# Kernel tuning notes

Measured on AMD Instinct MI355X. Metric: run time of the kernel, lower is better.

The kernel has to match this reference:

```python
import jax, jax.numpy as jnp
import numpy as np
from jax.scipy.linalg import expm

N = 8
FS = 48000
NFFT = FS * 8              # irfft length, hardcoded in the module
F = NFFT // 2 + 1          # one-sided spectrum length = 192001
GAIN_PER_SAMPLE = 0.9999
_DELAYS = np.array([809., 877., 937., 1049., 1151., 1249., 1373., 1499.], dtype=np.float32)
M_AVR = float(_DELAYS.mean())
M_STD = float(_DELAYS.std(ddof=1))  # torch.std is unbiased


def setup_inputs() -> dict:
    key = jax.random.key(0)
    kB, kC, kW = jax.random.split(key, 3)
    # frequency grid on the upper unit circle, z = e^{i w}, w in [0, pi]
    w = jnp.linspace(0.0, np.pi, F).astype(jnp.float32)
    x = jnp.exp(1j * w).astype(jnp.complex64)
    B = (jax.random.normal(kB, (N, 1), dtype=jnp.float32) / N)
    C = (jax.random.normal(kC, (N,), dtype=jnp.float32) / N)
    W = jax.random.normal(kW, (N, N), dtype=jnp.float32)  # seed for Skew+MatrixExponential parametrization
    m = jnp.asarray((_DELAYS - M_AVR) / M_STD)            # normalized delays (learnable)
    return {"x": x, "B": B, "C": C, "W": W, "m": m}


def reference(x, B, C, W, m):
    # A = expm(skew(W)), an orthogonal feedback matrix  [N,N]
    S = jnp.triu(W, 1)
    A = expm(S - S.T)
    # de-normalize delays
    md = m * M_STD + M_AVR                                # [N]
    gamma = jnp.power(GAIN_PER_SAMPLE, md)                # [N] real
    # D(z) = diag(z^m)  per frequency  -> [F,N] complex
    xm = jnp.power(x[:, None], md[None, :].astype(jnp.complex64))
    # M = D - A @ Gamma ; A @ diag(gamma) == A * gamma (column scaling)
    AG = (A * gamma[None, :]).astype(jnp.complex64)       # [N,N]
    eye = jnp.eye(N, dtype=jnp.complex64)
    Mmat = xm[:, None, :] * eye - AG[None, :, :]          # [F,N,N]
    # Hchannel = inv(M) @ B  (solved, same math as inverse+matmul)
    Bc = jnp.broadcast_to(B.astype(jnp.complex64), (F, N, 1))
    Hch = jnp.linalg.solve(Mmat, Bc)[:, :, 0]             # [F,N]
    H = Hch * C[None, :].astype(jnp.complex64)            # [F,N]
    Hsum = jnp.sum(H, axis=-1)                            # [F]
    mask = jnp.where(x == 0, 0.0, 1.0).astype(Hsum.real.dtype)
    h = jnp.fft.irfft(Hsum * mask, n=NFFT)                # [NFFT] real
    h = h / jnp.max(jnp.abs(h))
    return H, h
```

## Files before the change

kernel.cpp:

```cpp
#include <hip/hip_runtime.h>
#include <math.h>

#define F_LEN 192001
#define NFFT  384000
#define MHALF 192000
#define NCH   8

__device__ __forceinline__ float2 cmulf(float2 a, float2 b) {
  return make_float2(a.x*b.x - a.y*b.y, a.x*b.y + a.y*b.x);
}
__device__ __forceinline__ float2 caddf2(float2 a, float2 b){ return make_float2(a.x+b.x, a.y+b.y); }
__device__ __forceinline__ float2 csubf2(float2 a, float2 b){ return make_float2(a.x-b.x, a.y-b.y); }

__global__ __launch_bounds__(64) void precompute_kernel(
    const float* __restrict__ W, const float* __restrict__ m,
    double* __restrict__ md_d, float* __restrict__ AG, unsigned int* __restrict__ mxbits)
{
  __shared__ double S[64], P[64], T[64];
  __shared__ double norm_sh;
  const int t = threadIdx.x;
  const int i = t >> 3, j = t & 7;

  double wij = (j > i) ? (double)W[i*8+j] : 0.0;
  double wji = (i > j) ? (double)W[j*8+i] : 0.0;
  S[t] = wij - wji;
  __syncthreads();

  if (t == 0) {
    double best = 0.0;
    for (int r = 0; r < 8; ++r) {
      double rs = 0.0;
      for (int c = 0; c < 8; ++c) rs += fabs(S[r*8+c]);
      best = fmax(best, rs);
    }
    norm_sh = best;
  }
  __syncthreads();

  double nrm = norm_sh;
  int s = 0;
  while (nrm > 0.25 && s < 60) { nrm *= 0.5; ++s; }
  S[t] *= ldexp(1.0, -s);

  P[t] = (i == j) ? 1.0 : 0.0;
  T[t] = P[t];
  __syncthreads();

  for (int k = 1; k <= 24; ++k) {
    double acc = 0.0;
    #pragma unroll
    for (int l = 0; l < 8; ++l) acc += T[i*8+l] * S[l*8+j];
    __syncthreads();
    T[t] = acc / (double)k;
    P[t] += T[t];
    __syncthreads();
  }
  for (int q = 0; q < s; ++q) {
    double acc = 0.0;
    #pragma unroll
    for (int l = 0; l < 8; ++l) acc += P[i*8+l] * P[l*8+j];
    __syncthreads();
    P[t] = acc;
    __syncthreads();
  }

  const double M_AVR = 1118.0;
  const double M_STDd = (double)((float)sqrt(419520.0 / 7.0));
  const double LN_GAIN = log(0.9999);

  double md_j  = (double)m[j] * M_STDd + M_AVR;
  double gam_j = exp(md_j * LN_GAIN);
  AG[t] = (float)(P[t] * gam_j);

  if (t < 8) md_d[t] = (double)m[t] * M_STDd + M_AVR;
  if (t == 0) *mxbits = 0u;
}

__global__ __launch_bounds__(256) void freq_solve_kernel(
    const double* __restrict__ md_d, const float* __restrict__ AG,
    const float* __restrict__ Bp, const float* __restrict__ Cp,
    float* __restrict__ outH, float2* __restrict__ Y, int interleaved)
{
  int f = blockIdx.x * blockDim.x + threadIdx.x;
  if (f >= F_LEN) return;

  const double TWO_PI = 6.283185307179586476925287;
  double fd = (double)f;
  float xc[8], xs[8];
  #pragma unroll
  for (int n = 0; n < 8; ++n) {
    double tt = fd * md_d[n] * (1.0 / (double)NFFT);
    tt -= floor(tt);
    float ang = (float)(tt * TWO_PI);
    __sincosf(ang, &xs[n], &xc[n]);
  }

  float2 Mm[8][8];
  float2 yv[8];
  float2 idg[8];
  #pragma unroll
  for (int i = 0; i < 8; ++i) {
    #pragma unroll
    for (int j = 0; j < 8; ++j) {
      float2 v = make_float2(-AG[i*8+j], 0.0f);
      if (i == j) { v.x += xc[i]; v.y = xs[i]; }
      Mm[i][j] = v;
    }
    yv[i] = make_float2(Bp[i], 0.0f);
  }

  #pragma unroll
  for (int k = 0; k < 8; ++k) {
    float2 p = Mm[k][k];
    float rd = 1.0f / (p.x*p.x + p.y*p.y);
    float2 inv = make_float2(p.x*rd, -p.y*rd);
    idg[k] = inv;
    #pragma unroll
    for (int i = k+1; i < 8; ++i) {
      float2 fm = cmulf(Mm[i][k], inv);
      #pragma unroll
      for (int j = k+1; j < 8; ++j)
        Mm[i][j] = csubf2(Mm[i][j], cmulf(fm, Mm[k][j]));
      yv[i] = csubf2(yv[i], cmulf(fm, yv[k]));
    }
  }
  #pragma unroll
  for (int k = 7; k >= 0; --k) {
    float2 acc = yv[k];
    #pragma unroll
    for (int j = k+1; j < 8; ++j)
      acc = csubf2(acc, cmulf(Mm[k][j], yv[j]));
    yv[k] = cmulf(acc, idg[k]);
  }

  float2 hsum = make_float2(0.f, 0.f);
  #pragma unroll
  for (int n = 0; n < 8; ++n) {
    float c = Cp[n];
    float2 H = make_float2(yv[n].x * c, yv[n].y * c);
    yv[n] = H;
    hsum = caddf2(hsum, H);
  }

  if (interleaved) {
    float2* o = (float2*)outH;
    #pragma unroll
    for (int n = 0; n < 8; ++n) o[f*8+n] = yv[n];
  } else {
    #pragma unroll
    for (int n = 0; n < 8; ++n) outH[f*8+n] = yv[n].x;
  }

  Y[f] = hsum;
}

__device__ __forceinline__ void dft4_inv(float2* v) {
  float2 t0 = caddf2(v[0], v[2]);
  float2 t1 = csubf2(v[0], v[2]);
  float2 t2 = caddf2(v[1], v[3]);
  float2 t3 = csubf2(v[1], v[3]);
  float2 it3 = make_float2(-t3.y, t3.x);
  v[0] = caddf2(t0, t2);
  v[1] = caddf2(t1, it3);
  v[2] = csubf2(t0, t2);
  v[3] = csubf2(t1, it3);
}

__device__ __forceinline__ void dft3_inv(float2* v) {
  const float S3 = 0.86602540378443864676f;
  float2 t1 = caddf2(v[1], v[2]);
  float2 d  = csubf2(v[1], v[2]);
  float2 u  = make_float2(v[0].x - 0.5f*t1.x, v[0].y - 0.5f*t1.y);
  float2 idd = make_float2(-S3*d.y, S3*d.x);
  v[0] = caddf2(v[0], t1);
  v[1] = caddf2(u, idd);
  v[2] = csubf2(u, idd);
}

__device__ __forceinline__ void dft5_inv(float2* v) {
  const float C1 =  0.30901699437494742410f;
  const float S1 =  0.95105651629515357212f;
  const float C2 = -0.80901699437494742410f;
  const float S2 =  0.58778525229247312917f;
  float2 t1 = caddf2(v[1], v[4]);
  float2 t2 = caddf2(v[2], v[3]);
  float2 t3 = csubf2(v[1], v[4]);
  float2 t4 = csubf2(v[2], v[3]);
  float2 x0 = v[0];
  float2 a1 = make_float2(x0.x + C1*t1.x + C2*t2.x, x0.y + C1*t1.y + C2*t2.y);
  float2 b1 = make_float2(S1*t3.x + S2*t4.x,        S1*t3.y + S2*t4.y);
  float2 a2 = make_float2(x0.x + C2*t1.x + C1*t2.x, x0.y + C2*t1.y + C1*t2.y);
  float2 b2 = make_float2(S2*t3.x - S1*t4.x,        S2*t3.y - S1*t4.y);
  float2 ib1 = make_float2(-b1.y, b1.x);
  float2 ib2 = make_float2(-b2.y, b2.x);
  v[0] = make_float2(x0.x + t1.x + t2.x, x0.y + t1.y + t2.y);
  v[1] = caddf2(a1, ib1);
  v[4] = csubf2(a1, ib1);
  v[2] = caddf2(a2, ib2);
  v[3] = csubf2(a2, ib2);
}

__device__ __constant__ float TW25[25][2] = {
  { 1.0f, 0.0f },
  { 0.9685831611286311f,  0.2486898871648548f },
  { 0.8763066800438636f,  0.4817536741017153f },
  { 0.7289686274214116f,  0.6845471059286887f },
  { 0.5358267949789967f,  0.8443279255020151f },
  { 0.3090169943749474f,  0.9510565162951535f },
  { 0.0627905195293134f,  0.9980267284282716f },
  {-0.1873813145857246f,  0.9822872507286887f },
  {-0.4257792915650727f,  0.9048270524660196f },
  {-0.6374239897486896f,  0.7705132427757893f },
  {-0.8090169943749474f,  0.5877852522924731f },
  {-0.9297764858882515f,  0.3681245526846780f },
  {-0.9921147013144779f,  0.1253332335643043f },
  {-0.9921147013144779f, -0.1253332335643043f },
  {-0.9297764858882515f, -0.3681245526846780f },
  {-0.8090169943749474f, -0.5877852522924731f },
  {-0.6374239897486899f, -0.7705132427757891f },
  {-0.4257792915650727f, -0.9048270524660196f },
  {-0.1873813145857246f, -0.9822872507286887f },
  { 0.0627905195293134f, -0.9980267284282716f },
  { 0.3090169943749474f, -0.9510565162951535f },
  { 0.5358267949789967f, -0.8443279255020151f },
  { 0.7289686274214116f, -0.6845471059286887f },
  { 0.8763066800438636f, -0.4817536741017153f },
  { 0.9685831611286311f, -0.2486898871648548f },
};

template <int R>
__device__ __forceinline__ void dft_inv(float2* v) {
  if constexpr (R == 3) {
    dft3_inv(v);
  } else if constexpr (R == 4) {
    dft4_inv(v);
  } else if constexpr (R == 5) {
    dft5_inv(v);
  } else if constexpr (R == 8) {
    const float HF = 0.70710678118654752440f;
    float2 e[4] = {v[0], v[2], v[4], v[6]};
    float2 o[4] = {v[1], v[3], v[5], v[7]};
    dft4_inv(e); dft4_inv(o);
    o[1] = cmulf(o[1], make_float2(HF, HF));
    o[2] = make_float2(-o[2].y, o[2].x);
    o[3] = cmulf(o[3], make_float2(-HF, HF));
    #pragma unroll
    for (int k = 0; k < 4; ++k) {
      v[k]   = caddf2(e[k], o[k]);
      v[k+4] = csubf2(e[k], o[k]);
    }
  } else if constexpr (R == 15) {
    float2 a[5][3];
    #pragma unroll
    for (int n2 = 0; n2 < 5; ++n2) {
      #pragma unroll
      for (int n1 = 0; n1 < 3; ++n1)
        a[n2][n1] = v[(5*n1 + 3*n2) % 15];
      dft3_inv(a[n2]);
    }
    #pragma unroll
    for (int k1 = 0; k1 < 3; ++k1) {
      float2 b[5];
      #pragma unroll
      for (int n2 = 0; n2 < 5; ++n2) b[n2] = a[n2][k1];
      dft5_inv(b);
      #pragma unroll
      for (int k2 = 0; k2 < 5; ++k2) v[(10*k1 + 6*k2) % 15] = b[k2];
    }
  } else if constexpr (R == 25) {
    float2 a[5][5];
    #pragma unroll
    for (int n2 = 0; n2 < 5; ++n2) {
      float2 b[5];
      #pragma unroll
      for (int n1 = 0; n1 < 5; ++n1) b[n1] = v[5*n1 + n2];
      dft5_inv(b);
      #pragma unroll
      for (int k1 = 0; k1 < 5; ++k1) a[k1][n2] = b[k1];
    }
    #pragma unroll
    for (int k1 = 1; k1 < 5; ++k1) {
      #pragma unroll
      for (int n2 = 1; n2 < 5; ++n2) {
        const int mm = (n2 * k1) % 25;
        a[k1][n2] = cmulf(a[k1][n2], make_float2(TW25[mm][0], TW25[mm][1]));
      }
    }
    #pragma unroll
    for (int k1 = 0; k1 < 5; ++k1) {
      dft5_inv(a[k1]);
      #pragma unroll
      for (int k2 = 0; k2 < 5; ++k2) v[k1 + 5*k2] = a[k1][k2];
    }
  }
}

__global__ __launch_bounds__(256) void fft_first8(
    const float2* __restrict__ Y, float2* __restrict__ out)
{
  constexpr int NT = MHALF / 8;
  int j = blockIdx.x * blockDim.x + threadIdx.x;
  if (j >= NT) return;

  float2 v[8];
  #pragma unroll
  for (int r = 0; r < 8; ++r) {
    int t = j + r * NT;
    float2 Ya = Y[t];
    float2 Ym = Y[MHALF - t];
    if (t == 0) { Ya.y = 0.f; Ym.y = 0.f; }
    float2 E  = make_float2(Ya.x + Ym.x, Ya.y - Ym.y);
    float2 Oc = make_float2(Ya.x - Ym.x, Ya.y + Ym.y);
    double tt = (double)t * (1.0 / (double)NFFT);
    float ang = (float)(6.283185307179586476925287 * tt);
    float sn, cs; __sincosf(ang, &sn, &cs);
    float2 O = make_float2(cs*Oc.x - sn*Oc.y, cs*Oc.y + sn*Oc.x);
    v[r] = make_float2(E.x - O.y, E.y + O.x);
  }
  dft_inv<8>(v);
  int base = j * 8;
  #pragma unroll
  for (int r = 0; r < 8; ++r) out[base + r] = v[r];
}

template <int R, bool DOMAX>
__global__ __launch_bounds__(256) void fft_pass(
    const float2* __restrict__ in, float2* __restrict__ out, int Ns,
    unsigned int* __restrict__ mx)
{
  constexpr int NT = MHALF / R;
  int j = blockIdx.x * blockDim.x + threadIdx.x;
  if (j >= NT) return;
  int jm = j % Ns;
  int jd = j / Ns;

  float2 v[R];
  double tb = (double)jm / (double)(Ns * R);
  #pragma unroll
  for (int r = 0; r < R; ++r) {
    float2 x = in[j + r * NT];
    if (r > 0) {
      float ang = (float)(6.283185307179586476925287 * (tb * (double)r));
      float sn, cs; __sincosf(ang, &sn, &cs);
      x = cmulf(x, make_float2(cs, sn));
    }
    v[r] = x;
  }
  dft_inv<R>(v);
  int base = jd * (Ns * R) + jm;
  #pragma unroll
  for (int r = 0; r < R; ++r) out[base + r * Ns] = v[r];

  if constexpr (DOMAX) {
    float m = 0.f;
    #pragma unroll
    for (int r = 0; r < R; ++r)
      m = fmaxf(m, fmaxf(fabsf(v[r].x), fabsf(v[r].y)));
    #pragma unroll
    for (int off = 32; off > 0; off >>= 1)
      m = fmaxf(m, __shfl_xor(m, off));
    if ((threadIdx.x & 63) == 0) atomicMax(mx, __float_as_uint(m));
  }
}

__global__ __launch_bounds__(256) void norm_kernel(
    const float2* __restrict__ z, const unsigned int* __restrict__ mx,
    float2* __restrict__ hout)
{
  int n = blockIdx.x * blockDim.x + threadIdx.x;
  if (n >= MHALF) return;
  float mxv = __uint_as_float(*mx);
  float2 zz = z[n];
  hout[n] = make_float2(zz.x / mxv, zz.y / mxv);
}

extern "C" void kernel_launch(void* const* d_in, const int* in_sizes, int n_in,
                              void* d_out, int out_size, void* d_ws, size_t ws_size,
                              hipStream_t stream)
{
  const float* Bp = (const float*)d_in[1];
  const float* Cp = (const float*)d_in[2];
  const float* Wp = (const float*)d_in[3];
  const float* mp = (const float*)d_in[4];

  char* ws = (char*)d_ws;
  double* md_d = (double*)ws;
  float*  AG   = (float*)(ws + 64);
  unsigned int* mx = (unsigned int*)(ws + 384);
  float2* bufY = (float2*)(ws + 512);
  float2* bufA = (float2*)(ws + 512 + 1536128);
  float2* bufB = bufA + MHALF;

  float* outf = (float*)d_out;
  const int hoff = out_size - NFFT;
  const int interleaved = (hoff >= 2 * F_LEN * NCH) ? 1 : 0;

  precompute_kernel<<<1, 64, 0, stream>>>(Wp, mp, md_d, AG, mx);
  freq_solve_kernel<<<(F_LEN + 255) / 256, 256, 0, stream>>>(
      md_d, AG, Bp, Cp, outf, bufY, interleaved);

  fft_first8<<<(MHALF/8 + 255)/256, 256, 0, stream>>>(bufY, bufA);
  fft_pass<8,  false><<<(MHALF/8  + 255)/256, 256, 0, stream>>>(bufA, bufB, 8,    mx);
  fft_pass<8,  false><<<(MHALF/8  + 255)/256, 256, 0, stream>>>(bufB, bufA, 64,   mx);
  fft_pass<15, false><<<(MHALF/15 + 255)/256, 256, 0, stream>>>(bufA, bufB, 512,  mx);
  fft_pass<25, true ><<<(MHALF/25 + 255)/256, 256, 0, stream>>>(bufB, bufA, 7680, mx);

  norm_kernel<<<(MHALF + 255)/256, 256, 0, stream>>>(bufA, mx, (float2*)(outf + hoff));
}
```

Measured before the change: 43.51 us.

## Fuse five global FFT passes into two LDS-staged kernels, trim expm series

Replaces the five separate radix passes of the inverse real FFT with two kernels. The first does three radix-8 stages in shared memory per 512-point sub-FFT, and the second does the radix-15 and radix-25 stages in shared memory, which cuts global round trips and launch overhead. It also relaxes the expm scaling threshold and shortens the Taylor series from 24 to 13 terms, and vectorises the normalisation with a reciprocal multiply. The trade-offs are low grid parallelism (125 and 64 blocks, many idle threads in fftB) and slightly changed expm accuracy.

```diff
diff --git a/kernel.cpp b/kernel.cpp
--- a/kernel.cpp
+++ b/kernel.cpp
@@ -39,14 +39,14 @@
 
   double nrm = norm_sh;
   int s = 0;
-  while (nrm > 0.25 && s < 60) { nrm *= 0.5; ++s; }
+  while (nrm > 0.5 && s < 60) { nrm *= 0.5; ++s; }
   S[t] *= ldexp(1.0, -s);
 
   P[t] = (i == j) ? 1.0 : 0.0;
   T[t] = P[t];
   __syncthreads();
 
-  for (int k = 1; k <= 24; ++k) {
+  for (int k = 1; k <= 13; ++k) {
     double acc = 0.0;
     #pragma unroll
     for (int l = 0; l < 8; ++l) acc += T[i*8+l] * S[l*8+j];
@@ -198,6 +198,41 @@
   v[4] = csubf2(a1, ib1);
   v[2] = caddf2(a2, ib2);
   v[3] = csubf2(a2, ib2);
+}
+
+__device__ __forceinline__ void dft8_inv(float2* v) {
+  const float HF = 0.70710678118654752440f;
+  float2 e[4] = {v[0], v[2], v[4], v[6]};
+  float2 o[4] = {v[1], v[3], v[5], v[7]};
+  dft4_inv(e); dft4_inv(o);
+  o[1] = cmulf(o[1], make_float2(HF, HF));
+  o[2] = make_float2(-o[2].y, o[2].x);
+  o[3] = cmulf(o[3], make_float2(-HF, HF));
+  #pragma unroll
+  for (int k = 0; k < 4; ++k) {
+    v[k]   = caddf2(e[k], o[k]);
+    v[k+4] = csubf2(e[k], o[k]);
+  }
+}
+
+__device__ __forceinline__ void dft15_inv(float2* v) {
+  float2 a[5][3];
+  #pragma unroll
+  for (int n2 = 0; n2 < 5; ++n2) {
+    #pragma unroll
+    for (int n1 = 0; n1 < 3; ++n1)
+      a[n2][n1] = v[(5*n1 + 3*n2) % 15];
+    dft3_inv(a[n2]);
+  }
+  #pragma unroll
+  for (int k1 = 0; k1 < 3; ++k1) {
+    float2 b[5];
+    #pragma unroll
+    for (int n2 = 0; n2 < 5; ++n2) b[n2] = a[n2][k1];
+    dft5_inv(b);
+    #pragma unroll
+    for (int k2 = 0; k2 < 5; ++k2) v[(10*k1 + 6*k2) % 15] = b[k2];
+  }
 }
 
 __device__ __constant__ float TW25[25][2] = {
@@ -228,150 +263,181 @@
   { 0.9685831611286311f, -0.2486898871648548f },
 };
 
-template <int R>
-__device__ __forceinline__ void dft_inv(float2* v) {
-  if constexpr (R == 3) {
-    dft3_inv(v);
-  } else if constexpr (R == 4) {
-    dft4_inv(v);
-  } else if constexpr (R == 5) {
-    dft5_inv(v);
-  } else if constexpr (R == 8) {
-    const float HF = 0.70710678118654752440f;
-    float2 e[4] = {v[0], v[2], v[4], v[6]};
-    float2 o[4] = {v[1], v[3], v[5], v[7]};
-    dft4_inv(e); dft4_inv(o);
-    o[1] = cmulf(o[1], make_float2(HF, HF));
-    o[2] = make_float2(-o[2].y, o[2].x);
-    o[3] = cmulf(o[3], make_float2(-HF, HF));
-    #pragma unroll
-    for (int k = 0; k < 4; ++k) {
-      v[k]   = caddf2(e[k], o[k]);
-      v[k+4] = csubf2(e[k], o[k]);
-    }
-  } else if constexpr (R == 15) {
-    float2 a[5][3];
-    #pragma unroll
-    for (int n2 = 0; n2 < 5; ++n2) {
-      #pragma unroll
-      for (int n1 = 0; n1 < 3; ++n1)
-        a[n2][n1] = v[(5*n1 + 3*n2) % 15];
-      dft3_inv(a[n2]);
-    }
-    #pragma unroll
-    for (int k1 = 0; k1 < 3; ++k1) {
-      float2 b[5];
-      #pragma unroll
-      for (int n2 = 0; n2 < 5; ++n2) b[n2] = a[n2][k1];
-      dft5_inv(b);
-      #pragma unroll
-      for (int k2 = 0; k2 < 5; ++k2) v[(10*k1 + 6*k2) % 15] = b[k2];
-    }
-  } else if constexpr (R == 25) {
-    float2 a[5][5];
-    #pragma unroll
-    for (int n2 = 0; n2 < 5; ++n2) {
-      float2 b[5];
-      #pragma unroll
-      for (int n1 = 0; n1 < 5; ++n1) b[n1] = v[5*n1 + n2];
-      dft5_inv(b);
-      #pragma unroll
-      for (int k1 = 0; k1 < 5; ++k1) a[k1][n2] = b[k1];
-    }
-    #pragma unroll
-    for (int k1 = 1; k1 < 5; ++k1) {
-      #pragma unroll
-      for (int n2 = 1; n2 < 5; ++n2) {
-        const int mm = (n2 * k1) % 25;
-        a[k1][n2] = cmulf(a[k1][n2], make_float2(TW25[mm][0], TW25[mm][1]));
-      }
-    }
-    #pragma unroll
-    for (int k1 = 0; k1 < 5; ++k1) {
-      dft5_inv(a[k1]);
-      #pragma unroll
-      for (int k2 = 0; k2 < 5; ++k2) v[k1 + 5*k2] = a[k1][k2];
-    }
-  }
-}
-
-__global__ __launch_bounds__(256) void fft_first8(
+__device__ __forceinline__ void dft25_inv(float2* v) {
+  float2 a[5][5];
+  #pragma unroll
+  for (int n2 = 0; n2 < 5; ++n2) {
+    float2 b[5];
+    #pragma unroll
+    for (int n1 = 0; n1 < 5; ++n1) b[n1] = v[5*n1 + n2];
+    dft5_inv(b);
+    #pragma unroll
+    for (int k1 = 0; k1 < 5; ++k1) a[k1][n2] = b[k1];
+  }
+  #pragma unroll
+  for (int k1 = 1; k1 < 5; ++k1) {
+    #pragma unroll
+    for (int n2 = 1; n2 < 5; ++n2) {
+      const int mm = (n2 * k1) % 25;
+      a[k1][n2] = cmulf(a[k1][n2], make_float2(TW25[mm][0], TW25[mm][1]));
+    }
+  }
+  #pragma unroll
+  for (int k1 = 0; k1 < 5; ++k1) {
+    dft5_inv(a[k1]);
+    #pragma unroll
+    for (int k2 = 0; k2 < 5; ++k2) v[k1 + 5*k2] = a[k1][k2];
+  }
+}
+
+__global__ __launch_bounds__(192) void fftA_kernel(
     const float2* __restrict__ Y, float2* __restrict__ out)
 {
-  constexpr int NT = MHALF / 8;
-  int j = blockIdx.x * blockDim.x + threadIdx.x;
-  if (j >= NT) return;
+  __shared__ float2 lds[3][576];
+  const int wave = threadIdx.x >> 6;
+  const int l = threadIdx.x & 63;
+  const int d = blockIdx.x * 3 + wave;
+  float2* A = lds[wave];
+  const double TWO_PI = 6.283185307179586476925287;
 
   float2 v[8];
   #pragma unroll
   for (int r = 0; r < 8; ++r) {
-    int t = j + r * NT;
-    float2 Ya = Y[t];
-    float2 Ym = Y[MHALF - t];
-    if (t == 0) { Ya.y = 0.f; Ym.y = 0.f; }
+    int t = l + 64*r;
+    int n = d + 375*t;
+    float2 Ya = Y[n];
+    float2 Ym = Y[MHALF - n];
+    if (n == 0) { Ya.y = 0.f; Ym.y = 0.f; }
     float2 E  = make_float2(Ya.x + Ym.x, Ya.y - Ym.y);
     float2 Oc = make_float2(Ya.x - Ym.x, Ya.y + Ym.y);
-    double tt = (double)t * (1.0 / (double)NFFT);
-    float ang = (float)(6.283185307179586476925287 * tt);
+    double tt = (double)n * (1.0 / (double)NFFT);
+    float ang = (float)(TWO_PI * tt);
     float sn, cs; __sincosf(ang, &sn, &cs);
     float2 O = make_float2(cs*Oc.x - sn*Oc.y, cs*Oc.y + sn*Oc.x);
     v[r] = make_float2(E.x - O.y, E.y + O.x);
   }
-  dft_inv<8>(v);
-  int base = j * 8;
-  #pragma unroll
-  for (int r = 0; r < 8; ++r) out[base + r] = v[r];
-}
-
-template <int R, bool DOMAX>
-__global__ __launch_bounds__(256) void fft_pass(
-    const float2* __restrict__ in, float2* __restrict__ out, int Ns,
-    unsigned int* __restrict__ mx)
-{
-  constexpr int NT = MHALF / R;
-  int j = blockIdx.x * blockDim.x + threadIdx.x;
-  if (j >= NT) return;
-  int jm = j % Ns;
-  int jd = j / Ns;
-
-  float2 v[R];
-  double tb = (double)jm / (double)(Ns * R);
-  #pragma unroll
-  for (int r = 0; r < R; ++r) {
-    float2 x = in[j + r * NT];
-    if (r > 0) {
-      float ang = (float)(6.283185307179586476925287 * (tb * (double)r));
+  dft8_inv(v);
+  #pragma unroll
+  for (int r = 0; r < 8; ++r) { int idx = 8*l + r; A[idx + (idx>>3)] = v[r]; }
+  __syncthreads();
+
+  {
+    int jm = l & 7, jd = l >> 3;
+    #pragma unroll
+    for (int r = 0; r < 8; ++r) { int idx = l + 64*r; v[r] = A[idx + (idx>>3)]; }
+    double tb = (double)jm * (1.0/64.0);
+    #pragma unroll
+    for (int r = 1; r < 8; ++r) {
+      float ang = (float)(TWO_PI * tb * (double)r);
       float sn, cs; __sincosf(ang, &sn, &cs);
-      x = cmulf(x, make_float2(cs, sn));
-    }
-    v[r] = x;
-  }
-  dft_inv<R>(v);
-  int base = jd * (Ns * R) + jm;
-  #pragma unroll
-  for (int r = 0; r < R; ++r) out[base + r * Ns] = v[r];
-
-  if constexpr (DOMAX) {
-    float m = 0.f;
-    #pragma unroll
-    for (int r = 0; r < R; ++r)
-      m = fmaxf(m, fmaxf(fabsf(v[r].x), fabsf(v[r].y)));
-    #pragma unroll
-    for (int off = 32; off > 0; off >>= 1)
-      m = fmaxf(m, __shfl_xor(m, off));
-    if ((threadIdx.x & 63) == 0) atomicMax(mx, __float_as_uint(m));
-  }
+      v[r] = cmulf(v[r], make_float2(cs, sn));
+    }
+    dft8_inv(v);
+    __syncthreads();
+    #pragma unroll
+    for (int r = 0; r < 8; ++r) { int idx = jd*64 + jm + 8*r; A[idx + (idx>>3)] = v[r]; }
+  }
+  __syncthreads();
+
+  {
+    #pragma unroll
+    for (int r = 0; r < 8; ++r) { int idx = l + 64*r; v[r] = A[idx + (idx>>3)]; }
+    double tb = (double)l * (1.0/512.0);
+    #pragma unroll
+    for (int r = 1; r < 8; ++r) {
+      float ang = (float)(TWO_PI * tb * (double)r);
+      float sn, cs; __sincosf(ang, &sn, &cs);
+      v[r] = cmulf(v[r], make_float2(cs, sn));
+    }
+    dft8_inv(v);
+    #pragma unroll
+    for (int r = 0; r < 8; ++r) out[d*512 + l + 64*r] = v[r];
+  }
+}
+
+__global__ __launch_bounds__(256) void fftB_kernel(
+    const float2* __restrict__ Ain, float2* __restrict__ out, unsigned int* __restrict__ mx)
+{
+  __shared__ float2 lds[375*9];
+  const int tid = threadIdx.x;
+  const int J0 = blockIdx.x * 8;
+  const double TWO_PI = 6.283185307179586476925287;
+
+  #pragma unroll
+  for (int k = 0; k < 12; ++k) {
+    int i = tid + 256*k;
+    if (i < 3000) {
+      int d = i >> 3, jl = i & 7;
+      lds[d*9 + jl] = Ain[d*512 + J0 + jl];
+    }
+  }
+  __syncthreads();
+
+  {
+    bool act = tid < 200;
+    int jl = tid & 7, jd = tid >> 3;
+    float2 p[15];
+    if (act) {
+      #pragma unroll
+      for (int r = 0; r < 15; ++r) p[r] = lds[(jd + 25*r)*9 + jl];
+    }
+    __syncthreads();
+    if (act) {
+      int jm = J0 + jl;
+      double tb = (double)jm * (1.0/7680.0);
+      #pragma unroll
+      for (int r = 1; r < 15; ++r) {
+        float ang = (float)(TWO_PI * tb * (double)r);
+        float sn, cs; __sincosf(ang, &sn, &cs);
+        p[r] = cmulf(p[r], make_float2(cs, sn));
+      }
+      dft15_inv(p);
+      #pragma unroll
+      for (int r = 0; r < 15; ++r) lds[(15*jd + r)*9 + jl] = p[r];
+    }
+  }
+  __syncthreads();
+
+  float mloc = 0.f;
+  {
+    bool act = tid < 120;
+    int jl = tid & 7, s = tid >> 3;
+    float2 q[25];
+    if (act) {
+      #pragma unroll
+      for (int r = 0; r < 25; ++r) q[r] = lds[(s + 15*r)*9 + jl];
+      int jm = J0 + jl;
+      int j = jm + 512*s;
+      double tb = (double)j * (1.0/(double)MHALF);
+      #pragma unroll
+      for (int r = 1; r < 25; ++r) {
+        float ang = (float)(TWO_PI * tb * (double)r);
+        float sn, cs; __sincosf(ang, &sn, &cs);
+        q[r] = cmulf(q[r], make_float2(cs, sn));
+      }
+      dft25_inv(q);
+      #pragma unroll
+      for (int r = 0; r < 25; ++r) {
+        out[jm + 512*(s + 15*r)] = q[r];
+        mloc = fmaxf(mloc, fmaxf(fabsf(q[r].x), fabsf(q[r].y)));
+      }
+    }
+  }
+  #pragma unroll
+  for (int off = 32; off > 0; off >>= 1)
+    mloc = fmaxf(mloc, __shfl_xor(mloc, off));
+  if ((tid & 63) == 0) atomicMax(mx, __float_as_uint(mloc));
 }
 
 __global__ __launch_bounds__(256) void norm_kernel(
-    const float2* __restrict__ z, const unsigned int* __restrict__ mx,
-    float2* __restrict__ hout)
+    const float4* __restrict__ z, const unsigned int* __restrict__ mx,
+    float4* __restrict__ hout)
 {
   int n = blockIdx.x * blockDim.x + threadIdx.x;
-  if (n >= MHALF) return;
-  float mxv = __uint_as_float(*mx);
-  float2 zz = z[n];
-  hout[n] = make_float2(zz.x / mxv, zz.y / mxv);
+  if (n >= MHALF/2) return;
+  float r = 1.0f / __uint_as_float(*mx);
+  float4 zz = z[n];
+  hout[n] = make_float4(zz.x*r, zz.y*r, zz.z*r, zz.w*r);
 }
 
 extern "C" void kernel_launch(void* const* d_in, const int* in_sizes, int n_in,
@@ -399,11 +465,9 @@
   freq_solve_kernel<<<(F_LEN + 255) / 256, 256, 0, stream>>>(
       md_d, AG, Bp, Cp, outf, bufY, interleaved);
 
-  fft_first8<<<(MHALF/8 + 255)/256, 256, 0, stream>>>(bufY, bufA);
-  fft_pass<8,  false><<<(MHALF/8  + 255)/256, 256, 0, stream>>>(bufA, bufB, 8,    mx);
-  fft_pass<8,  false><<<(MHALF/8  + 255)/256, 256, 0, stream>>>(bufB, bufA, 64,   mx);
-  fft_pass<15, false><<<(MHALF/15 + 255)/256, 256, 0, stream>>>(bufA, bufB, 512,  mx);
-  fft_pass<25, true ><<<(MHALF/25 + 255)/256, 256, 0, stream>>>(bufB, bufA, 7680, mx);
-
-  norm_kernel<<<(MHALF + 255)/256, 256, 0, stream>>>(bufA, mx, (float2*)(outf + hoff));
-}
+  fftA_kernel<<<125, 192, 0, stream>>>(bufY, bufA);
+  fftB_kernel<<<64, 256, 0, stream>>>(bufA, bufB, mx);
+
+  norm_kernel<<<(MHALF/2 + 255)/256, 256, 0, stream>>>(
+      (const float4*)bufB, mx, (float4*)(outf + hoff));
+}
```

Result: faster. 37.58 us, median of 2 (-13.6%).
